# Optimization experiments

Measured on AMD Instinct MI355X. Metric: run time of the kernel, lower is better.

The kernel has to match this reference:

```python
import jax, jax.numpy as jnp
import numpy as np

N = 6144       # num nodes
F_IN = 256     # in_channels
HID = 64       # hidden
OUT = 64       # out_channels
E = 196608     # num edges (avg degree 32)
ALPHA = 0.8
EPS = 1e-6     # prob clamp (stand-in for torch clamp_probs tiny)
BN_EPS = 1e-5


def setup_inputs() -> dict:
    key = jax.random.key(0)
    ks = jax.random.split(key, 6)
    x = jax.random.normal(ks[0], (N, F_IN), jnp.float32)
    edge_index = jax.random.randint(ks[1], (2, E), 0, N, dtype=jnp.int64)
    W1 = jax.random.normal(ks[2], (F_IN, HID), jnp.float32) / np.float32(np.sqrt(F_IN))
    b1 = jnp.zeros((HID,), jnp.float32)
    W2 = jax.random.normal(ks[3], (HID, OUT), jnp.float32) / np.float32(np.sqrt(HID))
    b2 = jnp.zeros((OUT,), jnp.float32)
    gamma = jnp.ones((HID,), jnp.float32)
    beta = jnp.zeros((HID,), jnp.float32)
    prelu_a = jnp.full((1,), 0.25, jnp.float32)
    u = jax.random.uniform(ks[4], (N, N), jnp.float32, minval=1e-6, maxval=1.0 - 1e-6)
    return dict(x=x, edge_index=edge_index, W1=W1, b1=b1, W2=W2, b2=b2,
                gamma=gamma, beta=beta, prelu_a=prelu_a, u=u)


def _gcn_edge(x, src, dst, W, b, n):
    # PyG GCNConv: add self-loops, D^-1/2 (A+I) D^-1/2 (x W) + b
    h = x @ W
    loop = jnp.arange(n, dtype=src.dtype)
    src2 = jnp.concatenate([src, loop])
    dst2 = jnp.concatenate([dst, loop])
    deg = jax.ops.segment_sum(jnp.ones_like(src2, h.dtype), dst2, num_segments=n)
    dinv = jax.lax.rsqrt(deg)  # deg >= 1 due to self-loops
    norm = dinv[src2] * dinv[dst2]
    out = jax.ops.segment_sum(h[src2] * norm[:, None], dst2, num_segments=n)
    return out + b


def reference(x, edge_index, W1, b1, W2, b2, gamma, beta, prelu_a, u):
    n = x.shape[0]
    src, dst = edge_index[0], edge_index[1]

    # --- sample(alpha=0.8, x, edge_index) ---
    h = _gcn_edge(x, src, dst, W1, b1, n)                      # conv1 on original graph
    adj_orig = jnp.zeros((n, n), h.dtype).at[src, dst].set(1.0)  # directed scatter, as in the loop
    adj_logits = h @ h.T                                        # [N, N]
    edge_probs = ALPHA * (adj_logits / jnp.max(adj_logits)) + (1.0 - ALPHA) * adj_orig
    edge_probs = jnp.maximum(edge_probs, 0.0)                   # where(p<0, 0, p)
    p = jnp.clip(edge_probs, EPS, 1.0 - EPS)
    logits = jnp.log(p) - jnp.log1p(-p)
    noise = jnp.log(u) - jnp.log1p(-u)                          # logistic noise
    soft = jax.nn.sigmoid(logits + noise)                       # RelaxedBernoulli, temperature=1
    st = soft + jax.lax.stop_gradient(jnp.round(soft) - soft)   # straight-through hard sample
    a = jnp.triu(st, 1)
    a = a + a.T
    eye = jnp.eye(n, dtype=a.dtype)
    adj_sampled = a + eye                                       # fill_diagonal_(1) (triu(1) zeroed diag)

    # --- main conv stack on sampled graph (nonzero -> edge list -> GCNConv adds self-loops again) ---
    A = adj_sampled + eye                                       # diag weight becomes 2, faithful to PyG
    dinv = jax.lax.rsqrt(A.sum(axis=1))
    An = dinv[:, None] * A * dinv[None, :]
    x1 = An @ (x @ W1) + b1                                     # conv 0
    z = jnp.where(x1 >= 0, x1, prelu_a * x1)                    # PReLU
    mean = x1.mean(axis=0)
    var = x1.var(axis=0)                                        # biased, training-mode BN
    xb = gamma * (x1 - mean) * jax.lax.rsqrt(var + BN_EPS) + beta
    xr = jax.nn.relu(xb)                                        # dropout p=0 is a no-op
    x2 = An @ (xr @ W2) + b2                                    # conv 1
    return (x2, z, adj_sampled, adj_logits, adj_orig)
```

## Files before the change

### kernel.cpp

```cpp
#include <hip/hip_runtime.h>
#include <hip/hip_bf16.h>
#include <math.h>

#define NN 6144
#define FIN 256
#define HID 64


__global__ __launch_bounds__(256) void k_hxw(const float* __restrict__ x,
                                             const float* __restrict__ W1,
                                             double* __restrict__ hxw) {
  int t = blockIdx.x * 256 + threadIdx.x;
  int i = t >> 6, c = t & 63;
  const float* xr = x + (size_t)i * FIN;
  double a = 0.0;
#pragma unroll 8
  for (int k = 0; k < FIN; ++k)
    a = fma((double)xr[k], (double)W1[k * HID + c], a);
  hxw[t] = a;
}

__global__ __launch_bounds__(256) void k_edges(const int* __restrict__ ei, int E,
                                               int* __restrict__ deg,
                                               float* __restrict__ adjO) {
  int e = blockIdx.x * 256 + threadIdx.x;
  if (e >= E) return;
  int s = ei[e], d = ei[E + e];
  atomicAdd(&deg[d], 1);
  adjO[(size_t)s * NN + d] = 1.0f;
}

__global__ __launch_bounds__(256) void k_dinv(const int* __restrict__ deg,
                                              double* __restrict__ dinv) {
  int i = blockIdx.x * 256 + threadIdx.x;
  if (i < NN) dinv[i] = 1.0 / sqrt((double)(deg[i] + 1));
}

__global__ __launch_bounds__(256) void k_agg(const int* __restrict__ ei, int E,
                                             const double* __restrict__ hxw,
                                             const double* __restrict__ dinv,
                                             double* __restrict__ hagg) {
  int t = blockIdx.x * 256 + threadIdx.x;
  if (t >= E * HID) return;
  int e = t >> 6, c = t & 63;
  int s = ei[e], d = ei[E + e];
  atomicAdd(&hagg[(size_t)d * HID + c], hxw[(size_t)s * HID + c] * (dinv[s] * dinv[d]));
}

__global__ __launch_bounds__(256) void k_selfbias(const double* __restrict__ hxw,
                                                  const double* __restrict__ dinv,
                                                  const float* __restrict__ b1,
                                                  double* __restrict__ hagg) {
  int t = blockIdx.x * 256 + threadIdx.x;
  int i = t >> 6, c = t & 63;
  hagg[t] += hxw[t] * dinv[i] * dinv[i] + (double)b1[c];
}

__global__ __launch_bounds__(256) void k_lmax(const double* __restrict__ h,
                                              unsigned long long* __restrict__ lmax) {
  __shared__ double red[256];
  int i = blockIdx.x * 256 + threadIdx.x;
  const double* hr = h + (size_t)i * HID;
  double s = 0.0;
  for (int c = 0; c < HID; ++c) s = fma(hr[c], hr[c], s);
  red[threadIdx.x] = s;
  __syncthreads();
  for (int w = 128; w > 0; w >>= 1) {
    if (threadIdx.x < w) {
      double o = red[threadIdx.x + w];
      if (o > red[threadIdx.x]) red[threadIdx.x] = o;
    }
    __syncthreads();
  }
  if (threadIdx.x == 0)
    atomicMax(lmax, (unsigned long long)__double_as_longlong(red[0]));
}

__global__ __launch_bounds__(256) void k_tile(const double* __restrict__ h,
                                              const unsigned long long* __restrict__ lmaxp,
                                              const float* __restrict__ u,
                                              const float* __restrict__ adjO,
                                              float* __restrict__ adjL,
                                              float* __restrict__ adjS) {
  int I = blockIdx.y, J = blockIdx.x;
  if (J < I) return;
  __shared__ double smem[2 * 64 * 33];
  double* As = smem;
  double* Bs = smem + 64 * 33;
  float* Ls = (float*)smem;
  float* Ss = ((float*)smem) + 64 * 65;
  int t = threadIdx.x;
  int tx = t & 15, ty = t >> 4;
  double acc[4][4];
#pragma unroll
  for (int p = 0; p < 4; ++p)
#pragma unroll
    for (int q = 0; q < 4; ++q) acc[p][q] = 0.0;
  const double* hI = h + (size_t)I * 64 * HID;
  const double* hJ = h + (size_t)J * 64 * HID;
  for (int k0 = 0; k0 < 64; k0 += 32) {
    __syncthreads();
    for (int idx = t; idx < 2048; idx += 256) {
      int r = idx >> 5, k = idx & 31;
      As[r * 33 + k] = hI[r * 64 + k0 + k];
      Bs[r * 33 + k] = hJ[r * 64 + k0 + k];
    }
    __syncthreads();
#pragma unroll 8
    for (int k = 0; k < 32; ++k) {
      double a0 = As[ty * 33 + k], a1 = As[(ty + 16) * 33 + k];
      double a2 = As[(ty + 32) * 33 + k], a3 = As[(ty + 48) * 33 + k];
      double c0 = Bs[tx * 33 + k], c1 = Bs[(tx + 16) * 33 + k];
      double c2 = Bs[(tx + 32) * 33 + k], c3 = Bs[(tx + 48) * 33 + k];
      acc[0][0] = fma(a0, c0, acc[0][0]); acc[0][1] = fma(a0, c1, acc[0][1]);
      acc[0][2] = fma(a0, c2, acc[0][2]); acc[0][3] = fma(a0, c3, acc[0][3]);
      acc[1][0] = fma(a1, c0, acc[1][0]); acc[1][1] = fma(a1, c1, acc[1][1]);
      acc[1][2] = fma(a1, c2, acc[1][2]); acc[1][3] = fma(a1, c3, acc[1][3]);
      acc[2][0] = fma(a2, c0, acc[2][0]); acc[2][1] = fma(a2, c1, acc[2][1]);
      acc[2][2] = fma(a2, c2, acc[2][2]); acc[2][3] = fma(a2, c3, acc[2][3]);
      acc[3][0] = fma(a3, c0, acc[3][0]); acc[3][1] = fma(a3, c1, acc[3][1]);
      acc[3][2] = fma(a3, c2, acc[3][2]); acc[3][3] = fma(a3, c3, acc[3][3]);
    }
  }
  __syncthreads();
  double Lmax = __longlong_as_double((long long)(*lmaxp));
  bool diag = (I == J);
#pragma unroll
  for (int p = 0; p < 4; ++p) {
#pragma unroll
    for (int q = 0; q < 4; ++q) {
      int r = ty + 16 * p, c = tx + 16 * q;
      int gi = I * 64 + r, gj = J * 64 + c;
      double L = acc[p][q];
      float lf = (float)L;
      adjL[(size_t)gi * NN + gj] = lf;
      float stv;
      if (diag && r == c) {
        stv = 1.0f;
      } else {
        size_t ab = (gi < gj) ? ((size_t)gi * NN + gj) : ((size_t)gj * NN + gi);
        double ao = (double)adjO[ab];
        double uu = (double)u[ab];
        double ep = 0.8 * (L / Lmax) + 0.2 * ao;
        if (ep < 0.0) ep = 0.0;
        double pl = ep;
        if (pl < 1e-6) pl = 1e-6;
        double hi = 1.0 - 1e-6;
        if (pl > hi) pl = hi;
        stv = (pl > 1.0 - uu) ? 1.0f : 0.0f;
      }
      adjS[(size_t)gi * NN + gj] = stv;
      if (!diag) {
        Ls[c * 65 + r] = lf;
        Ss[c * 65 + r] = stv;
      }
    }
  }
  if (!diag) {
    __syncthreads();
    for (int idx = t; idx < 4096; idx += 256) {
      int a = idx >> 6, b = idx & 63;
      size_t off = (size_t)(J * 64 + a) * NN + (I * 64 + b);
      adjL[off] = Ls[a * 65 + b];
      adjS[off] = Ss[a * 65 + b];
    }
  }
}

__global__ __launch_bounds__(256) void k_rowsum(const float* __restrict__ adjS,
                                                double* __restrict__ dinv2) {
  __shared__ int red[256];
  int i = blockIdx.x;
  int cnt = 0;
  for (int j = threadIdx.x; j < NN; j += 256)
    cnt += (adjS[(size_t)i * NN + j] > 0.5f) ? 1 : 0;
  red[threadIdx.x] = cnt;
  __syncthreads();
  for (int w = 128; w > 0; w >>= 1) {
    if (threadIdx.x < w) red[threadIdx.x] += red[threadIdx.x + w];
    __syncthreads();
  }
  if (threadIdx.x == 0) dinv2[i] = 1.0 / sqrt((double)(red[0] + 1));
}

__global__ __launch_bounds__(256) void k_gscale(const double* __restrict__ hv,
                                                const double* __restrict__ dinv2,
                                                float* __restrict__ g) {
  int t = blockIdx.x * 256 + threadIdx.x;
  int j = t >> 6;
  g[t] = (float)(dinv2[j] * hv[t]);
}

__global__ __launch_bounds__(256) void k_anmm(const float* __restrict__ adjS,
                                              const float* __restrict__ g,
                                              float* __restrict__ accb) {
  int I = blockIdx.x;
  int s = blockIdx.y;
  __shared__ float as[64 * 65];
  __shared__ float gs[64 * 64];
  int t = threadIdx.x, tx = t & 15, ty = t >> 4;
  float acc[4][4];
#pragma unroll
  for (int p = 0; p < 4; ++p)
#pragma unroll
    for (int q = 0; q < 4; ++q) acc[p][q] = 0.0f;
  for (int Jt = s * 12; Jt < (s + 1) * 12; ++Jt) {
    __syncthreads();
    for (int idx = t; idx < 4096; idx += 256) {
      int r = idx >> 6, cc = idx & 63;
      as[r * 65 + cc] = adjS[(size_t)(I * 64 + r) * NN + Jt * 64 + cc];
      gs[idx] = g[(size_t)(Jt * 64 + r) * HID + cc];
    }
    __syncthreads();
#pragma unroll 4
    for (int j = 0; j < 64; ++j) {
      float c0 = gs[j * 64 + tx], c1 = gs[j * 64 + tx + 16];
      float c2 = gs[j * 64 + tx + 32], c3 = gs[j * 64 + tx + 48];
      float a0 = as[ty * 65 + j], a1 = as[(ty + 16) * 65 + j];
      float a2 = as[(ty + 32) * 65 + j], a3 = as[(ty + 48) * 65 + j];
      acc[0][0] = fmaf(a0, c0, acc[0][0]); acc[0][1] = fmaf(a0, c1, acc[0][1]);
      acc[0][2] = fmaf(a0, c2, acc[0][2]); acc[0][3] = fmaf(a0, c3, acc[0][3]);
      acc[1][0] = fmaf(a1, c0, acc[1][0]); acc[1][1] = fmaf(a1, c1, acc[1][1]);
      acc[1][2] = fmaf(a1, c2, acc[1][2]); acc[1][3] = fmaf(a1, c3, acc[1][3]);
      acc[2][0] = fmaf(a2, c0, acc[2][0]); acc[2][1] = fmaf(a2, c1, acc[2][1]);
      acc[2][2] = fmaf(a2, c2, acc[2][2]); acc[2][3] = fmaf(a2, c3, acc[2][3]);
      acc[3][0] = fmaf(a3, c0, acc[3][0]); acc[3][1] = fmaf(a3, c1, acc[3][1]);
      acc[3][2] = fmaf(a3, c2, acc[3][2]); acc[3][3] = fmaf(a3, c3, acc[3][3]);
    }
  }
  float* out = accb + (size_t)s * NN * HID;
#pragma unroll
  for (int p = 0; p < 4; ++p)
#pragma unroll
    for (int q = 0; q < 4; ++q)
      out[(size_t)(I * 64 + ty + 16 * p) * HID + tx + 16 * q] = acc[p][q];
}

__global__ __launch_bounds__(256) void k_ep1(const float* __restrict__ accb,
                                             const float* __restrict__ g,
                                             const double* __restrict__ dinv2,
                                             const float* __restrict__ b1,
                                             const float* __restrict__ prelu,
                                             float* __restrict__ x1,
                                             float* __restrict__ zout) {
  int t = blockIdx.x * 256 + threadIdx.x;
  int i = t >> 6, c = t & 63;
  double ss = 0.0;
  for (int s = 0; s < 8; ++s) ss += (double)accb[(size_t)s * NN * HID + t];
  float v = (float)(dinv2[i] * (ss + (double)g[t])) + b1[c];
  x1[t] = v;
  float pa = prelu[0];
  zout[t] = v >= 0.0f ? v : pa * v;
}

__global__ __launch_bounds__(256) void k_bnstats(const float* __restrict__ x1,
                                                 double* __restrict__ meanv,
                                                 double* __restrict__ istd) {
  __shared__ double r1[256], r2[256];
  int c = blockIdx.x;
  double s1 = 0.0, s2 = 0.0;
  for (int i = threadIdx.x; i < NN; i += 256) {
    double v = (double)x1[(size_t)i * HID + c];
    s1 += v;
    s2 += v * v;
  }
  r1[threadIdx.x] = s1;
  r2[threadIdx.x] = s2;
  __syncthreads();
  for (int w = 128; w > 0; w >>= 1) {
    if (threadIdx.x < w) {
      r1[threadIdx.x] += r1[threadIdx.x + w];
      r2[threadIdx.x] += r2[threadIdx.x + w];
    }
    __syncthreads();
  }
  if (threadIdx.x == 0) {
    double m = r1[0] / (double)NN;
    double var = r2[0] / (double)NN - m * m;
    meanv[c] = m;
    istd[c] = 1.0 / sqrt(var + 1e-5);
  }
}

__global__ __launch_bounds__(256) void k_xr(const float* __restrict__ x1,
                                            const double* __restrict__ meanv,
                                            const double* __restrict__ istd,
                                            const float* __restrict__ gamma,
                                            const float* __restrict__ beta,
                                            float* __restrict__ xr) {
  int t = blockIdx.x * 256 + threadIdx.x;
  int c = t & 63;
  float v = gamma[c] * (float)(((double)x1[t] - meanv[c]) * istd[c]) + beta[c];
  xr[t] = v > 0.0f ? v : 0.0f;
}

__global__ __launch_bounds__(256) void k_y_g2(const float* __restrict__ xr,
                                              const float* __restrict__ W2,
                                              const double* __restrict__ dinv2,
                                              float* __restrict__ g2) {
  int t = blockIdx.x * 256 + threadIdx.x;
  int j = t >> 6, c = t & 63;
  const float* xrow = xr + (size_t)j * HID;
  float a = 0.0f;
#pragma unroll 8
  for (int k = 0; k < HID; ++k) a = fmaf(xrow[k], W2[k * HID + c], a);
  g2[t] = (float)(dinv2[j] * (double)a);
}

__global__ __launch_bounds__(256) void k_ep2(const float* __restrict__ accb,
                                             const float* __restrict__ g2,
                                             const double* __restrict__ dinv2,
                                             const float* __restrict__ b2p,
                                             float* __restrict__ x2out) {
  int t = blockIdx.x * 256 + threadIdx.x;
  int i = t >> 6, c = t & 63;
  double ss = 0.0;
  for (int s = 0; s < 8; ++s) ss += (double)accb[(size_t)s * NN * HID + t];
  x2out[t] = (float)(dinv2[i] * (ss + (double)g2[t])) + b2p[c];
}

extern "C" void kernel_launch(void* const* d_in, const int* in_sizes, int n_in,
                              void* d_out, int out_size, void* d_ws, size_t ws_size,
                              hipStream_t stream) {
  const float* x = (const float*)d_in[0];
  const int* ei = (const int*)d_in[1];
  const float* W1 = (const float*)d_in[2];
  const float* b1 = (const float*)d_in[3];
  const float* W2 = (const float*)d_in[4];
  const float* b2 = (const float*)d_in[5];
  const float* gamma = (const float*)d_in[6];
  const float* beta = (const float*)d_in[7];
  const float* prelu = (const float*)d_in[8];
  const float* u = (const float*)d_in[9];
  int E = in_sizes[1] / 2;

  float* out = (float*)d_out;
  float* o_x2 = out;
  float* o_z = out + (size_t)NN * HID;
  float* o_adjS = out + (size_t)2 * NN * HID;
  float* o_adjL = o_adjS + (size_t)NN * NN;
  float* o_adjO = o_adjL + (size_t)NN * NN;

  char* w = (char*)d_ws;
  double* hxw = (double*)w;
  double* hagg = (double*)(w + 3145728);
  double* dinv = (double*)(w + 6291456);
  int* deg = (int*)(w + 6340608);
  float* accb = (float*)w;
  double* dinv2 = (double*)(w + 12582912);
  unsigned long long* lmax = (unsigned long long*)(w + 12632064);
  double* meanv = (double*)(w + 12632128);
  double* istd = (double*)(w + 12632640);
  float* x1 = (float*)(w + 12633152);
  float* gg = (float*)(w + 14206016);
  float* xr = (float*)(w + 15778880);
  float* g2 = (float*)(w + 17351744);

  hipMemsetAsync(deg, 0, NN * sizeof(int), stream);
  hipMemsetAsync(hagg, 0, (size_t)NN * HID * sizeof(double), stream);
  hipMemsetAsync(lmax, 0, sizeof(unsigned long long), stream);
  hipMemsetAsync(o_adjO, 0, (size_t)NN * NN * sizeof(float), stream);

  k_hxw<<<NN * HID / 256, 256, 0, stream>>>(x, W1, hxw);
  k_edges<<<(E + 255) / 256, 256, 0, stream>>>(ei, E, deg, o_adjO);
  k_dinv<<<NN / 256, 256, 0, stream>>>(deg, dinv);
  k_agg<<<(E * HID + 255) / 256, 256, 0, stream>>>(ei, E, hxw, dinv, hagg);
  k_selfbias<<<NN * HID / 256, 256, 0, stream>>>(hxw, dinv, b1, hagg);
  k_lmax<<<NN / 256, 256, 0, stream>>>(hagg, lmax);
  dim3 gt(96, 96);
  k_tile<<<gt, 256, 0, stream>>>(hagg, lmax, u, o_adjO, o_adjL, o_adjS);
  k_rowsum<<<NN, 256, 0, stream>>>(o_adjS, dinv2);
  k_gscale<<<NN * HID / 256, 256, 0, stream>>>(hxw, dinv2, gg);
  dim3 ga(96, 8);
  k_anmm<<<ga, 256, 0, stream>>>(o_adjS, gg, accb);
  k_ep1<<<NN * HID / 256, 256, 0, stream>>>(accb, gg, dinv2, b1, prelu, x1, o_z);
  k_bnstats<<<HID, 256, 0, stream>>>(x1, meanv, istd);
  k_xr<<<NN * HID / 256, 256, 0, stream>>>(x1, meanv, istd, gamma, beta, xr);
  k_y_g2<<<NN * HID / 256, 256, 0, stream>>>(xr, W2, dinv2, g2);
  k_anmm<<<ga, 256, 0, stream>>>(o_adjS, g2, accb);
  k_ep2<<<NN * HID / 256, 256, 0, stream>>>(accb, g2, dinv2, b2, o_x2);
}
```

Baseline: 1.070 ms.

## Pack original and sampled adjacency into bitmasks for tile, rowsum and aggregation

Builds a bitmask copy of the original adjacency with atomicOr in the edge kernel, and has the tile kernel build a bitmask of the sampled adjacency using wavefront ballots. Row degree counting then uses popcount over 96 words per row, and both dense aggregation GEMMs read bits instead of the float NxN sampled matrix, which cuts the repeated full-matrix float reads. It also vectorizes the transposed stores and the g loads with float4. The cost is extra atomics and ballot work, and bitO reuses workspace that is later used for x1, so correctness depends on that ordering.

```diff
diff --git a/kernel.cpp b/kernel.cpp
--- a/kernel.cpp
+++ b/kernel.cpp
@@ -1,10 +1,11 @@
 #include <hip/hip_runtime.h>
-#include <hip/hip_bf16.h>
 #include <math.h>
 
 #define NN 6144
 #define FIN 256
 #define HID 64
+#define NW 96
+typedef unsigned long long u64;
 
 
 __global__ __launch_bounds__(256) void k_hxw(const float* __restrict__ x,
@@ -22,12 +23,14 @@
 
 __global__ __launch_bounds__(256) void k_edges(const int* __restrict__ ei, int E,
                                                int* __restrict__ deg,
-                                               float* __restrict__ adjO) {
+                                               float* __restrict__ adjO,
+                                               u64* __restrict__ bitO) {
   int e = blockIdx.x * 256 + threadIdx.x;
   if (e >= E) return;
   int s = ei[e], d = ei[E + e];
   atomicAdd(&deg[d], 1);
   adjO[(size_t)s * NN + d] = 1.0f;
+  atomicOr(&bitO[(size_t)s * NW + (d >> 6)], 1ull << (d & 63));
 }
 
 __global__ __launch_bounds__(256) void k_dinv(const int* __restrict__ deg,
@@ -57,7 +60,7 @@
 }
 
 __global__ __launch_bounds__(256) void k_lmax(const double* __restrict__ h,
-                                              unsigned long long* __restrict__ lmax) {
+                                              u64* __restrict__ lmax) {
   __shared__ double red[256];
   int i = blockIdx.x * 256 + threadIdx.x;
   const double* hr = h + (size_t)i * HID;
@@ -73,22 +76,23 @@
     __syncthreads();
   }
   if (threadIdx.x == 0)
-    atomicMax(lmax, (unsigned long long)__double_as_longlong(red[0]));
+    atomicMax(lmax, (u64)__double_as_longlong(red[0]));
 }
 
 __global__ __launch_bounds__(256) void k_tile(const double* __restrict__ h,
-                                              const unsigned long long* __restrict__ lmaxp,
+                                              const u64* __restrict__ lmaxp,
                                               const float* __restrict__ u,
-                                              const float* __restrict__ adjO,
+                                              const u64* __restrict__ bitO,
                                               float* __restrict__ adjL,
-                                              float* __restrict__ adjS) {
+                                              float* __restrict__ adjS,
+                                              u64* __restrict__ bitS) {
   int I = blockIdx.y, J = blockIdx.x;
   if (J < I) return;
-  __shared__ double smem[2 * 64 * 33];
+  __shared__ __align__(16) double smem[64 * 68];
   double* As = smem;
   double* Bs = smem + 64 * 33;
   float* Ls = (float*)smem;
-  float* Ss = ((float*)smem) + 64 * 65;
+  float* Ss = ((float*)smem) + 64 * 68;
   int t = threadIdx.x;
   int tx = t & 15, ty = t >> 4;
   double acc[4][4];
@@ -127,10 +131,13 @@
   bool diag = (I == J);
 #pragma unroll
   for (int p = 0; p < 4; ++p) {
+    int r = ty + 16 * p;
+    int gi = I * 64 + r;
+    float sv[4];
 #pragma unroll
     for (int q = 0; q < 4; ++q) {
-      int r = ty + 16 * p, c = tx + 16 * q;
-      int gi = I * 64 + r, gj = J * 64 + c;
+      int c = tx + 16 * q;
+      int gj = J * 64 + c;
       double L = acc[p][q];
       float lf = (float)L;
       adjL[(size_t)gi * NN + gj] = lf;
@@ -138,9 +145,10 @@
       if (diag && r == c) {
         stv = 1.0f;
       } else {
-        size_t ab = (gi < gj) ? ((size_t)gi * NN + gj) : ((size_t)gj * NN + gi);
-        double ao = (double)adjO[ab];
+        int ga = gi < gj ? gi : gj, gb = gi < gj ? gj : gi;
+        size_t ab = (size_t)ga * NN + gb;
         double uu = (double)u[ab];
+        double ao = (double)(int)((bitO[(size_t)ga * NW + (gb >> 6)] >> (gb & 63)) & 1ull);
         double ep = 0.8 * (L / Lmax) + 0.2 * ao;
         if (ep < 0.0) ep = 0.0;
         double pl = ep;
@@ -149,38 +157,46 @@
         if (pl > hi) pl = hi;
         stv = (pl > 1.0 - uu) ? 1.0f : 0.0f;
       }
+      sv[q] = stv;
       adjS[(size_t)gi * NN + gj] = stv;
       if (!diag) {
-        Ls[c * 65 + r] = lf;
-        Ss[c * 65 + r] = stv;
+        Ls[c * 68 + r] = lf;
+        Ss[c * 68 + r] = stv;
       }
     }
+    u64 word = 0;
+#pragma unroll
+    for (int q = 0; q < 4; ++q) {
+      u64 m = __ballot(sv[q] > 0.5f);
+      word |= ((m >> ((ty & 3) * 16)) & 0xFFFFull) << (16 * q);
+    }
+    if (tx == 0) bitS[(size_t)gi * NW + J] = word;
   }
   if (!diag) {
     __syncthreads();
-    for (int idx = t; idx < 4096; idx += 256) {
+    for (int i4 = t; i4 < 1024; i4 += 256) {
+      int a = i4 >> 4, b4 = (i4 & 15) << 2;
+      size_t off = (size_t)(J * 64 + a) * NN + (I * 64 + b4);
+      *(float4*)(adjL + off) = *(const float4*)&Ls[a * 68 + b4];
+      *(float4*)(adjS + off) = *(const float4*)&Ss[a * 68 + b4];
+    }
+    for (int k2 = 0; k2 < 16; ++k2) {
+      int idx = t + (k2 << 8);
       int a = idx >> 6, b = idx & 63;
-      size_t off = (size_t)(J * 64 + a) * NN + (I * 64 + b);
-      adjL[off] = Ls[a * 65 + b];
-      adjS[off] = Ss[a * 65 + b];
-    }
-  }
-}
-
-__global__ __launch_bounds__(256) void k_rowsum(const float* __restrict__ adjS,
-                                                double* __restrict__ dinv2) {
-  __shared__ int red[256];
-  int i = blockIdx.x;
+      u64 m = __ballot(Ss[a * 68 + b] > 0.5f);
+      if ((t & 63) == 0) bitS[(size_t)(J * 64 + a) * NW + I] = m;
+    }
+  }
+}
+
+__global__ __launch_bounds__(256) void k_rowsumB(const u64* __restrict__ bitS,
+                                                 double* __restrict__ dinv2) {
+  int i = blockIdx.x * 256 + threadIdx.x;
+  const u64* row = bitS + (size_t)i * NW;
   int cnt = 0;
-  for (int j = threadIdx.x; j < NN; j += 256)
-    cnt += (adjS[(size_t)i * NN + j] > 0.5f) ? 1 : 0;
-  red[threadIdx.x] = cnt;
-  __syncthreads();
-  for (int w = 128; w > 0; w >>= 1) {
-    if (threadIdx.x < w) red[threadIdx.x] += red[threadIdx.x + w];
-    __syncthreads();
-  }
-  if (threadIdx.x == 0) dinv2[i] = 1.0 / sqrt((double)(red[0] + 1));
+#pragma unroll
+  for (int wdx = 0; wdx < NW; ++wdx) cnt += __popcll(row[wdx]);
+  dinv2[i] = 1.0 / sqrt((double)(cnt + 1));
 }
 
 __global__ __launch_bounds__(256) void k_gscale(const double* __restrict__ hv,
@@ -191,13 +207,13 @@
   g[t] = (float)(dinv2[j] * hv[t]);
 }
 
-__global__ __launch_bounds__(256) void k_anmm(const float* __restrict__ adjS,
+__global__ __launch_bounds__(256) void k_anmm(const u64* __restrict__ bitS,
                                               const float* __restrict__ g,
                                               float* __restrict__ accb) {
   int I = blockIdx.x;
   int s = blockIdx.y;
-  __shared__ float as[64 * 65];
-  __shared__ float gs[64 * 64];
+  __shared__ __align__(16) float as[64 * 65];
+  __shared__ __align__(16) float gs[64 * 64];
   int t = threadIdx.x, tx = t & 15, ty = t >> 4;
   float acc[4][4];
 #pragma unroll
@@ -206,34 +222,37 @@
     for (int q = 0; q < 4; ++q) acc[p][q] = 0.0f;
   for (int Jt = s * 12; Jt < (s + 1) * 12; ++Jt) {
     __syncthreads();
+    for (int i4 = t; i4 < 1024; i4 += 256) {
+      int r = i4 >> 4, c4 = (i4 & 15) << 2;
+      *(float4*)&gs[r * 64 + c4] = *(const float4*)&g[(size_t)(Jt * 64 + r) * HID + c4];
+    }
     for (int idx = t; idx < 4096; idx += 256) {
       int r = idx >> 6, cc = idx & 63;
-      as[r * 65 + cc] = adjS[(size_t)(I * 64 + r) * NN + Jt * 64 + cc];
-      gs[idx] = g[(size_t)(Jt * 64 + r) * HID + cc];
+      u64 w = bitS[(size_t)(I * 64 + r) * NW + Jt];
+      as[r * 65 + cc] = (float)((w >> cc) & 1ull);
     }
     __syncthreads();
 #pragma unroll 4
     for (int j = 0; j < 64; ++j) {
-      float c0 = gs[j * 64 + tx], c1 = gs[j * 64 + tx + 16];
-      float c2 = gs[j * 64 + tx + 32], c3 = gs[j * 64 + tx + 48];
+      float4 cv = *(const float4*)&gs[j * 64 + (tx << 2)];
       float a0 = as[ty * 65 + j], a1 = as[(ty + 16) * 65 + j];
       float a2 = as[(ty + 32) * 65 + j], a3 = as[(ty + 48) * 65 + j];
-      acc[0][0] = fmaf(a0, c0, acc[0][0]); acc[0][1] = fmaf(a0, c1, acc[0][1]);
-      acc[0][2] = fmaf(a0, c2, acc[0][2]); acc[0][3] = fmaf(a0, c3, acc[0][3]);
-      acc[1][0] = fmaf(a1, c0, acc[1][0]); acc[1][1] = fmaf(a1, c1, acc[1][1]);
-      acc[1][2] = fmaf(a1, c2, acc[1][2]); acc[1][3] = fmaf(a1, c3, acc[1][3]);
-      acc[2][0] = fmaf(a2, c0, acc[2][0]); acc[2][1] = fmaf(a2, c1, acc[2][1]);
-      acc[2][2] = fmaf(a2, c2, acc[2][2]); acc[2][3] = fmaf(a2, c3, acc[2][3]);
-      acc[3][0] = fmaf(a3, c0, acc[3][0]); acc[3][1] = fmaf(a3, c1, acc[3][1]);
-      acc[3][2] = fmaf(a3, c2, acc[3][2]); acc[3][3] = fmaf(a3, c3, acc[3][3]);
+      acc[0][0] = fmaf(a0, cv.x, acc[0][0]); acc[0][1] = fmaf(a0, cv.y, acc[0][1]);
+      acc[0][2] = fmaf(a0, cv.z, acc[0][2]); acc[0][3] = fmaf(a0, cv.w, acc[0][3]);
+      acc[1][0] = fmaf(a1, cv.x, acc[1][0]); acc[1][1] = fmaf(a1, cv.y, acc[1][1]);
+      acc[1][2] = fmaf(a1, cv.z, acc[1][2]); acc[1][3] = fmaf(a1, cv.w, acc[1][3]);
+      acc[2][0] = fmaf(a2, cv.x, acc[2][0]); acc[2][1] = fmaf(a2, cv.y, acc[2][1]);
+      acc[2][2] = fmaf(a2, cv.z, acc[2][2]); acc[2][3] = fmaf(a2, cv.w, acc[2][3]);
+      acc[3][0] = fmaf(a3, cv.x, acc[3][0]); acc[3][1] = fmaf(a3, cv.y, acc[3][1]);
+      acc[3][2] = fmaf(a3, cv.z, acc[3][2]); acc[3][3] = fmaf(a3, cv.w, acc[3][3]);
     }
   }
   float* out = accb + (size_t)s * NN * HID;
 #pragma unroll
-  for (int p = 0; p < 4; ++p)
-#pragma unroll
-    for (int q = 0; q < 4; ++q)
-      out[(size_t)(I * 64 + ty + 16 * p) * HID + tx + 16 * q] = acc[p][q];
+  for (int p = 0; p < 4; ++p) {
+    float4 v = make_float4(acc[p][0], acc[p][1], acc[p][2], acc[p][3]);
+    *(float4*)&out[(size_t)(I * 64 + ty + 16 * p) * HID + (tx << 2)] = v;
+  }
 }
 
 __global__ __launch_bounds__(256) void k_ep1(const float* __restrict__ accb,
@@ -348,35 +367,38 @@
   int* deg = (int*)(w + 6340608);
   float* accb = (float*)w;
   double* dinv2 = (double*)(w + 12582912);
-  unsigned long long* lmax = (unsigned long long*)(w + 12632064);
+  u64* lmax = (u64*)(w + 12632064);
   double* meanv = (double*)(w + 12632128);
   double* istd = (double*)(w + 12632640);
   float* x1 = (float*)(w + 12633152);
   float* gg = (float*)(w + 14206016);
   float* xr = (float*)(w + 15778880);
   float* g2 = (float*)(w + 17351744);
+  u64* bitO = (u64*)(w + 12633152);
+  u64* bitS = (u64*)(w + 18924608);
 
   hipMemsetAsync(deg, 0, NN * sizeof(int), stream);
   hipMemsetAsync(hagg, 0, (size_t)NN * HID * sizeof(double), stream);
-  hipMemsetAsync(lmax, 0, sizeof(unsigned long long), stream);
+  hipMemsetAsync(lmax, 0, sizeof(u64), stream);
+  hipMemsetAsync(bitO, 0, (size_t)NN * NW * sizeof(u64), stream);
   hipMemsetAsync(o_adjO, 0, (size_t)NN * NN * sizeof(float), stream);
 
   k_hxw<<<NN * HID / 256, 256, 0, stream>>>(x, W1, hxw);
-  k_edges<<<(E + 255) / 256, 256, 0, stream>>>(ei, E, deg, o_adjO);
+  k_edges<<<(E + 255) / 256, 256, 0, stream>>>(ei, E, deg, o_adjO, bitO);
   k_dinv<<<NN / 256, 256, 0, stream>>>(deg, dinv);
   k_agg<<<(E * HID + 255) / 256, 256, 0, stream>>>(ei, E, hxw, dinv, hagg);
   k_selfbias<<<NN * HID / 256, 256, 0, stream>>>(hxw, dinv, b1, hagg);
   k_lmax<<<NN / 256, 256, 0, stream>>>(hagg, lmax);
   dim3 gt(96, 96);
-  k_tile<<<gt, 256, 0, stream>>>(hagg, lmax, u, o_adjO, o_adjL, o_adjS);
-  k_rowsum<<<NN, 256, 0, stream>>>(o_adjS, dinv2);
+  k_tile<<<gt, 256, 0, stream>>>(hagg, lmax, u, bitO, o_adjL, o_adjS, bitS);
+  k_rowsumB<<<NN / 256, 256, 0, stream>>>(bitS, dinv2);
   k_gscale<<<NN * HID / 256, 256, 0, stream>>>(hxw, dinv2, gg);
   dim3 ga(96, 8);
-  k_anmm<<<ga, 256, 0, stream>>>(o_adjS, gg, accb);
+  k_anmm<<<ga, 256, 0, stream>>>(bitS, gg, accb);
   k_ep1<<<NN * HID / 256, 256, 0, stream>>>(accb, gg, dinv2, b1, prelu, x1, o_z);
   k_bnstats<<<HID, 256, 0, stream>>>(x1, meanv, istd);
   k_xr<<<NN * HID / 256, 256, 0, stream>>>(x1, meanv, istd, gamma, beta, xr);
   k_y_g2<<<NN * HID / 256, 256, 0, stream>>>(xr, W2, dinv2, g2);
-  k_anmm<<<ga, 256, 0, stream>>>(o_adjS, g2, accb);
+  k_anmm<<<ga, 256, 0, stream>>>(bitS, g2, accb);
   k_ep2<<<NN * HID / 256, 256, 0, stream>>>(accb, g2, dinv2, b2, o_x2);
 }
```

Result: no change. 1.058 ms (-1.2%).
